# Kernel optimization log

Measured on AMD Instinct MI355X. Metric: run time of the kernel, lower is better.

The kernel has to match this reference:

```python
import jax, jax.numpy as jnp
import numpy as np

N_BLOCKS = 8
N_WIRES = 24
GAMMA, BETA, ALPHA = 0.1, 0.6, 0.15


def _apply_ry(state, w, theta):
    # RY(theta) = [[cos(t/2), -sin(t/2)], [sin(t/2), cos(t/2)]] on wire w.
    c = jnp.cos(theta * 0.5)
    s = jnp.sin(theta * 0.5)
    st = jnp.moveaxis(state, w, 0)  # (2, ...)
    new = jnp.stack([c * st[0] - s * st[1], s * st[0] + c * st[1]])
    return jnp.moveaxis(new, 0, w)


def _apply_cnot(state, ctrl, tgt):
    # Flip target bit where control bit == 1.
    st = jnp.moveaxis(state, (ctrl, tgt), (0, 1))  # (2, 2, ...)
    new = jnp.stack([st[0], st[1, ::-1]])
    return jnp.moveaxis(new, (0, 1), (ctrl, tgt))


def setup_inputs() -> dict:
    key = jax.random.key(0)
    angles = jax.random.normal(key, (N_BLOCKS, N_WIRES), dtype=jnp.float32)
    return {"angles": angles}


def reference(angles):
    n_blocks, n_wires = angles.shape  # static
    # Initial state |0...0>; RY and CNOT are real, so the state stays real.
    state = jnp.zeros((2,) * n_wires, dtype=angles.dtype).at[(0,) * n_wires].set(1.0)
    for k in range(n_blocks):
        for w in range(n_wires):
            state = _apply_ry(state, w, angles[k, w])
        for w in range(n_wires - 1):  # circular=False -> linear chain
            state = _apply_cnot(state, w, w + 1)
    probs = (state.reshape(-1) ** 2).reshape(2 ** n_wires, 1)  # |amp|^2
    easy_scale = 2.0 ** (n_wires - 1)
    x = (BETA * jnp.tanh(GAMMA * easy_scale * probs)) ** ALPHA
    return x - jnp.mean(x)
```

## Files before the change

kernel.cpp:

```cpp
#include <hip/hip_runtime.h>

#define NB 8
#define SSIZE (1u << 24)


__global__ void k_prep(const float* __restrict__ ang, float* __restrict__ ws) {
    int t = threadIdx.x;
    if (t == 0) ws[0] = 0.0f;
    if (t < NB * 24) {
        float a = 0.5f * ang[t];
        ws[64 + t]  = __builtin_cosf(a);
        ws[256 + t] = __builtin_sinf(a);
    }
}


__device__ __forceinline__ unsigned sw(unsigned f) {
    return f ^ (((f >> 3) ^ (f >> 5)) & 7u);
}

__device__ __forceinline__ void ry2(float& a0, float& a1, float c, float s, bool ctl) {
    float w0 = c * a0 - s * a1;
    float w1 = s * a0 + c * a1;
    a0 = ctl ? w1 : w0;
    a1 = ctl ? w0 : w1;
}

template<int TB, int MODE>
__device__ __forceinline__ void stage16(float4* x, float c, float s) {
#pragma unroll
    for (int j0 = 0; j0 < 16; ++j0) {
        if (j0 & (1 << TB)) continue;
        const int j1 = j0 | (1 << TB);
        const bool ctl = (MODE == 1) || (MODE == 0 && ((j0 >> (TB + 1)) & 1));
        ry2(x[j0].x, x[j1].x, c, s, ctl);
        ry2(x[j0].y, x[j1].y, c, s, ctl);
        ry2(x[j0].z, x[j1].z, c, s, ctl);
        ry2(x[j0].w, x[j1].w, c, s, ctl);
    }
}

__device__ __forceinline__ void dstages(float4* x, float c1, float s1,
                                        float c0, float s0) {
#pragma unroll
    for (int j = 0; j < 16; ++j) {
        bool ctl = j & 1;
        ry2(x[j].x, x[j].z, c1, s1, ctl);
        ry2(x[j].y, x[j].w, c1, s1, ctl);
        ry2(x[j].x, x[j].y, c0, s0, false);
        ry2(x[j].z, x[j].w, c0, s0, true);
    }
}

__device__ __forceinline__ float xform(float v) {
    float z = 838860.8f * v * v;
    float e2 = __builtin_amdgcn_exp2f(z * 2.8853900817779268f);
    float big = 1.0f - 2.0f * __builtin_amdgcn_rcpf(e2 + 1.0f);
    float z2 = z * z;
    float small_ = z * (1.0f - 0.33333333f * z2 * (1.0f - 0.4f * z2));
    float t = (z < 0.04f) ? small_ : big;
    return __builtin_amdgcn_exp2f(0.15f * __builtin_amdgcn_logf(0.6f * t));
}

__global__ __launch_bounds__(256, 2) void k_passA(float* __restrict__ st,
                                                  float* __restrict__ ws,
                                                  int k, int fuse) {
    __shared__ float4 T4[4096];
    const unsigned m = blockIdx.x;
    const unsigned tid = threadIdx.x;
    const float* C = ws + 64 + k * 24;
    const float* S = ws + 256 + k * 24;
    float ca[14], sa[14];
#pragma unroll
    for (int b = 0; b < 14; ++b) { ca[b] = C[23 - b]; sa[b] = S[23 - b]; }

    float4* G4 = reinterpret_cast<float4*>(st) + (m << 12);
    float4 x[16];

#pragma unroll
    for (int jj = 0; jj < 16; ++jj) x[jj] = G4[tid + (jj << 8)];
    if (m & 1u) stage16<3, 1>(x, ca[13], sa[13]);
    else        stage16<3,-1>(x, ca[13], sa[13]);
    stage16<2, 0>(x, ca[12], sa[12]);
    stage16<1, 0>(x, ca[11], sa[11]);
    stage16<0, 0>(x, ca[10], sa[10]);
#pragma unroll
    for (int jj = 0; jj < 16; ++jj) T4[sw(tid | (jj << 8))] = x[jj];
    __syncthreads();
    {
        const unsigned fb = (tid & 31) | ((tid >> 5) << 9);
#pragma unroll
        for (int jj = 0; jj < 16; ++jj) x[jj] = T4[sw(fb | (jj << 5))];
        stage16<2, 0>(x, ca[9], sa[9]);
        stage16<1, 0>(x, ca[8], sa[8]);
        stage16<0, 0>(x, ca[7], sa[7]);
#pragma unroll
        for (int jj = 0; jj < 16; ++jj) T4[sw(fb | (jj << 5))] = x[jj];
    }
    __syncthreads();
    {
        const unsigned fb = (tid & 3) | ((tid >> 2) << 6);
#pragma unroll
        for (int jj = 0; jj < 16; ++jj) x[jj] = T4[sw(fb | (jj << 2))];
        stage16<2, 0>(x, ca[6], sa[6]);
        stage16<1, 0>(x, ca[5], sa[5]);
        stage16<0, 0>(x, ca[4], sa[4]);
#pragma unroll
        for (int jj = 0; jj < 16; ++jj) T4[sw(fb | (jj << 2))] = x[jj];
    }
    __syncthreads();
    {
#pragma unroll
        for (int jj = 0; jj < 16; ++jj)
            x[jj] = T4[sw((jj & 7) | (tid << 3) | ((jj >> 3) << 11))];
        stage16<1, 0>(x, ca[3], sa[3]);
        stage16<0, 0>(x, ca[2], sa[2]);
        dstages(x, ca[1], sa[1], ca[0], sa[0]);
        if (fuse) {
            float lsum = 0.f;
#pragma unroll
            for (int jj = 0; jj < 16; ++jj) {
                float* v = &x[jj].x;
#pragma unroll
                for (int d = 0; d < 4; ++d) { v[d] = xform(v[d]); lsum += v[d]; }
            }
#pragma unroll
            for (int jj = 0; jj < 16; ++jj)
                G4[(jj & 7) | (tid << 3) | ((jj >> 3) << 11)] = x[jj];
#pragma unroll
            for (int o = 32; o > 0; o >>= 1) lsum += __shfl_down(lsum, o, 64);
            __syncthreads();
            float* wsum = reinterpret_cast<float*>(T4);
            if ((tid & 63u) == 0) wsum[tid >> 6] = lsum;
            __syncthreads();
            if (tid == 0)
                atomicAdd(ws, wsum[0] + wsum[1] + wsum[2] + wsum[3]);
        } else {
#pragma unroll
            for (int jj = 0; jj < 16; ++jj)
                G4[(jj & 7) | (tid << 3) | ((jj >> 3) << 11)] = x[jj];
        }
    }
}

__global__ __launch_bounds__(256, 2) void k_passB(float* __restrict__ st,
                                                  const float* __restrict__ ws,
                                                  int k, int init) {
    __shared__ float4 T4[4096];
    const unsigned m = blockIdx.x;
    const unsigned tid = threadIdx.x;
    const float* C = ws + 64 + k * 24;
    const float* S = ws + 256 + k * 24;
    float cg[10], sg[10];
#pragma unroll
    for (int t = 0; t < 10; ++t) { cg[t] = C[9 - t]; sg[t] = S[9 - t]; }

    float4* G4 = reinterpret_cast<float4*>(st);
    const unsigned mb = m << 2;
    float4 x[16];

    if (init) {
        const float* C0 = ws + 64;
        const float* S0 = ws + 256;
        unsigned t2 = tid & 3u;
        unsigned th = tid >> 2;
        float P = 1.f;
        { unsigned g = (t2 ^ (t2 >> 1)) & 1u;      P *= g ? S0[21] : C0[21]; }
        { unsigned g = ((t2 >> 1) ^ m) & 1u;       P *= g ? S0[20] : C0[20]; }
#pragma unroll
        for (int b = 4; b <= 12; ++b) {
            unsigned g = ((m >> (b - 4)) ^ (m >> (b - 3))) & 1u;
            P *= g ? S0[23 - b] : C0[23 - b];
        }
        { unsigned g = ((m >> 9) ^ th) & 1u;       P *= g ? S0[10] : C0[10]; }
#pragma unroll
        for (int b = 14; b <= 18; ++b) {
            unsigned g = ((th >> (b - 14)) ^ (th >> (b - 13))) & 1u;
            P *= g ? S0[23 - b] : C0[23 - b];
        }
        float D[4];
#pragma unroll
        for (int d = 0; d < 4; ++d) {
            unsigned g0 = (d ^ (d >> 1)) & 1u;
            unsigned g1 = ((d >> 1) ^ t2) & 1u;
            D[d] = (g0 ? S0[23] : C0[23]) * (g1 ? S0[22] : C0[22]);
        }
        unsigned th5 = (th >> 5) & 1u;
#pragma unroll
        for (int jj = 0; jj < 16; ++jj) {
            unsigned g19 = (th5 ^ (unsigned)jj) & 1u;
            unsigned g20 = ((unsigned)jj ^ ((unsigned)jj >> 1)) & 1u;
            unsigned g21 = (((unsigned)jj >> 1) ^ ((unsigned)jj >> 2)) & 1u;
            unsigned g22 = (((unsigned)jj >> 2) ^ ((unsigned)jj >> 3)) & 1u;
            unsigned g23 = ((unsigned)jj >> 3) & 1u;
            float J = (g19 ? S0[4] : C0[4]) * (g20 ? S0[3] : C0[3]) *
                      (g21 ? S0[2] : C0[2]) * (g22 ? S0[1] : C0[1]) *
                      (g23 ? S0[0] : C0[0]);
            float PJ = P * J;
            x[jj] = make_float4(PJ * D[0], PJ * D[1], PJ * D[2], PJ * D[3]);
        }
    } else {
#pragma unroll
        for (int jj = 0; jj < 16; ++jj) {
            unsigned lf = tid | (jj << 8);
            x[jj] = G4[((lf >> 2) << 12) | mb | (lf & 3u)];
        }
    }
    stage16<3,-1>(x, cg[9], sg[9]);
    stage16<2, 0>(x, cg[8], sg[8]);
    stage16<1, 0>(x, cg[7], sg[7]);
    stage16<0, 0>(x, cg[6], sg[6]);
#pragma unroll
    for (int jj = 0; jj < 16; ++jj) T4[sw(tid | (jj << 8))] = x[jj];
    __syncthreads();
    {
        const unsigned fb = (tid & 31) | ((tid >> 5) << 9);
#pragma unroll
        for (int jj = 0; jj < 16; ++jj) x[jj] = T4[sw(fb | (jj << 5))];
        stage16<2, 0>(x, cg[5], sg[5]);
        stage16<1, 0>(x, cg[4], sg[4]);
        stage16<0, 0>(x, cg[3], sg[3]);
#pragma unroll
        for (int jj = 0; jj < 16; ++jj) T4[sw(fb | (jj << 5))] = x[jj];
    }
    __syncthreads();
    {
        const unsigned fb = (tid & 3) | ((tid >> 2) << 6);
#pragma unroll
        for (int jj = 0; jj < 16; ++jj) x[jj] = T4[sw(fb | (jj << 2))];
        stage16<2, 0>(x, cg[2], sg[2]);
        stage16<1, 0>(x, cg[1], sg[1]);
        stage16<0, 0>(x, cg[0], sg[0]);
#pragma unroll
        for (int jj = 0; jj < 16; ++jj) {
            unsigned lf = fb | (jj << 2);
            G4[((lf >> 2) << 12) | mb | (lf & 3u)] = x[jj];
        }
    }
}

__global__ void k_final(float* __restrict__ st, const float* __restrict__ ws) {
    unsigned idx = blockIdx.x * blockDim.x + threadIdx.x;
    unsigned stride = gridDim.x * blockDim.x;
    float mean = ws[0] * (1.0f / 16777216.0f);
    float4* G4 = reinterpret_cast<float4*>(st);
    for (unsigned q = idx; q < (SSIZE / 4); q += stride) {
        float4 v = G4[q];
        v.x -= mean; v.y -= mean; v.z -= mean; v.w -= mean;
        G4[q] = v;
    }
}

extern "C" void kernel_launch(void* const* d_in, const int* in_sizes, int n_in,
                              void* d_out, int out_size, void* d_ws, size_t ws_size,
                              hipStream_t stream) {
    const float* ang = (const float*)d_in[0];
    float* st = (float*)d_out;
    float* ws = (float*)d_ws;

    k_prep<<<1, 256, 0, stream>>>(ang, ws);
    for (int k = 1; k < NB; ++k) {
        k_passB<<<1024, 256, 0, stream>>>(st, ws, k, (k == 1) ? 1 : 0);
        k_passA<<<1024, 256, 0, stream>>>(st, ws, k, (k == NB - 1) ? 1 : 0);
    }
    k_final<<<4096, 256, 0, stream>>>(st, ws);
}
```

Baseline: 613.1 us.

## Use 512-thread blocks with cross-lane shuffle stages instead of LDS transposes

Each pass now runs 512 threads per block, each holding 8 float4 instead of 16. Most of the former shared-memory transpose rounds are replaced by wave-level __shfl_xor butterfly stages, with per-lane coefficients encoding the RY and CNOT permutation. This cuts LDS traffic and __syncthreads barriers and lowers register pressure to raise occupancy. The cost is many more shuffle instructions and more complex index and coefficient bookkeeping.

```diff
diff --git a/kernel.cpp b/kernel.cpp
--- a/kernel.cpp
+++ b/kernel.cpp
@@ -27,9 +27,9 @@
 }
 
 template<int TB, int MODE>
-__device__ __forceinline__ void stage16(float4* x, float c, float s) {
-#pragma unroll
-    for (int j0 = 0; j0 < 16; ++j0) {
+__device__ __forceinline__ void stage8(float4* x, float c, float s) {
+#pragma unroll
+    for (int j0 = 0; j0 < 8; ++j0) {
         if (j0 & (1 << TB)) continue;
         const int j1 = j0 | (1 << TB);
         const bool ctl = (MODE == 1) || (MODE == 0 && ((j0 >> (TB + 1)) & 1));
@@ -40,13 +40,51 @@
     }
 }
 
-__device__ __forceinline__ void dstages(float4* x, float c1, float s1,
+__device__ __forceinline__ void coefs(unsigned lane, int lb, bool g,
+                                      float c, float s, float& cA, float& cP) {
+    bool b = (lane >> lb) & 1u;
+    cA = g ? (b ? -s : s) : c;
+    cP = g ? c : (b ? s : -s);
+}
+
+__device__ __forceinline__ void lane_stage(float4* x, int mask, float cA, float cP) {
+#pragma unroll
+    for (int j = 0; j < 8; ++j) {
+        float px = __shfl_xor(x[j].x, mask, 64);
+        float py = __shfl_xor(x[j].y, mask, 64);
+        float pz = __shfl_xor(x[j].z, mask, 64);
+        float pw = __shfl_xor(x[j].w, mask, 64);
+        x[j].x = cA * x[j].x + cP * px;
+        x[j].y = cA * x[j].y + cP * py;
+        x[j].z = cA * x[j].z + cP * pz;
+        x[j].w = cA * x[j].w + cP * pw;
+    }
+}
+
+__device__ __forceinline__ void lane_stage_jc(float4* x, int mask,
+                                              float cA0, float cP0,
+                                              float cA1, float cP1) {
+#pragma unroll
+    for (int j = 0; j < 8; ++j) {
+        float cA = (j & 1) ? cA1 : cA0;
+        float cP = (j & 1) ? cP1 : cP0;
+        float px = __shfl_xor(x[j].x, mask, 64);
+        float py = __shfl_xor(x[j].y, mask, 64);
+        float pz = __shfl_xor(x[j].z, mask, 64);
+        float pw = __shfl_xor(x[j].w, mask, 64);
+        x[j].x = cA * x[j].x + cP * px;
+        x[j].y = cA * x[j].y + cP * py;
+        x[j].z = cA * x[j].z + cP * pz;
+        x[j].w = cA * x[j].w + cP * pw;
+    }
+}
+
+__device__ __forceinline__ void dstages(float4* x, float c1, float s1, bool g1,
                                         float c0, float s0) {
 #pragma unroll
-    for (int j = 0; j < 16; ++j) {
-        bool ctl = j & 1;
-        ry2(x[j].x, x[j].z, c1, s1, ctl);
-        ry2(x[j].y, x[j].w, c1, s1, ctl);
+    for (int j = 0; j < 8; ++j) {
+        ry2(x[j].x, x[j].z, c1, s1, g1);
+        ry2(x[j].y, x[j].w, c1, s1, g1);
         ry2(x[j].x, x[j].y, c0, s0, false);
         ry2(x[j].z, x[j].w, c0, s0, true);
     }
@@ -62,12 +100,13 @@
     return __builtin_amdgcn_exp2f(0.15f * __builtin_amdgcn_logf(0.6f * t));
 }
 
-__global__ __launch_bounds__(256, 2) void k_passA(float* __restrict__ st,
+__global__ __launch_bounds__(512, 4) void k_passA(float* __restrict__ st,
                                                   float* __restrict__ ws,
                                                   int k, int fuse) {
     __shared__ float4 T4[4096];
     const unsigned m = blockIdx.x;
     const unsigned tid = threadIdx.x;
+    const unsigned lane = tid & 63u;
     const float* C = ws + 64 + k * 24;
     const float* S = ws + 256 + k * 24;
     float ca[14], sa[14];
@@ -75,80 +114,72 @@
     for (int b = 0; b < 14; ++b) { ca[b] = C[23 - b]; sa[b] = S[23 - b]; }
 
     float4* G4 = reinterpret_cast<float4*>(st) + (m << 12);
-    float4 x[16];
-
-#pragma unroll
-    for (int jj = 0; jj < 16; ++jj) x[jj] = G4[tid + (jj << 8)];
-    if (m & 1u) stage16<3, 1>(x, ca[13], sa[13]);
-    else        stage16<3,-1>(x, ca[13], sa[13]);
-    stage16<2, 0>(x, ca[12], sa[12]);
-    stage16<1, 0>(x, ca[11], sa[11]);
-    stage16<0, 0>(x, ca[10], sa[10]);
-#pragma unroll
-    for (int jj = 0; jj < 16; ++jj) T4[sw(tid | (jj << 8))] = x[jj];
+    float4 x[8];
+
+#pragma unroll
+    for (int jj = 0; jj < 8; ++jj) x[jj] = G4[tid + (jj << 9)];
+    if (m & 1u) stage8<2, 1>(x, ca[13], sa[13]);
+    else        stage8<2,-1>(x, ca[13], sa[13]);
+    stage8<1, 0>(x, ca[12], sa[12]);
+    stage8<0, 0>(x, ca[11], sa[11]);
+#pragma unroll
+    for (int jj = 0; jj < 8; ++jj) T4[sw(tid | (jj << 9))] = x[jj];
     __syncthreads();
+    const unsigned hi = (tid >> 6) << 9;
+#pragma unroll
+    for (int jj = 0; jj < 8; ++jj) x[jj] = T4[sw(lane | (jj << 6) | hi)];
+    if (tid & 64u) stage8<2, 1>(x, ca[10], sa[10]);
+    else           stage8<2,-1>(x, ca[10], sa[10]);
+    stage8<1, 0>(x, ca[9], sa[9]);
+    stage8<0, 0>(x, ca[8], sa[8]);
     {
-        const unsigned fb = (tid & 31) | ((tid >> 5) << 9);
-#pragma unroll
-        for (int jj = 0; jj < 16; ++jj) x[jj] = T4[sw(fb | (jj << 5))];
-        stage16<2, 0>(x, ca[9], sa[9]);
-        stage16<1, 0>(x, ca[8], sa[8]);
-        stage16<0, 0>(x, ca[7], sa[7]);
-#pragma unroll
-        for (int jj = 0; jj < 16; ++jj) T4[sw(fb | (jj << 5))] = x[jj];
-    }
-    __syncthreads();
-    {
-        const unsigned fb = (tid & 3) | ((tid >> 2) << 6);
-#pragma unroll
-        for (int jj = 0; jj < 16; ++jj) x[jj] = T4[sw(fb | (jj << 2))];
-        stage16<2, 0>(x, ca[6], sa[6]);
-        stage16<1, 0>(x, ca[5], sa[5]);
-        stage16<0, 0>(x, ca[4], sa[4]);
-#pragma unroll
-        for (int jj = 0; jj < 16; ++jj) T4[sw(fb | (jj << 2))] = x[jj];
-    }
-    __syncthreads();
-    {
-#pragma unroll
-        for (int jj = 0; jj < 16; ++jj)
-            x[jj] = T4[sw((jj & 7) | (tid << 3) | ((jj >> 3) << 11))];
-        stage16<1, 0>(x, ca[3], sa[3]);
-        stage16<0, 0>(x, ca[2], sa[2]);
-        dstages(x, ca[1], sa[1], ca[0], sa[0]);
-        if (fuse) {
-            float lsum = 0.f;
-#pragma unroll
-            for (int jj = 0; jj < 16; ++jj) {
-                float* v = &x[jj].x;
-#pragma unroll
-                for (int d = 0; d < 4; ++d) { v[d] = xform(v[d]); lsum += v[d]; }
-            }
-#pragma unroll
-            for (int jj = 0; jj < 16; ++jj)
-                G4[(jj & 7) | (tid << 3) | ((jj >> 3) << 11)] = x[jj];
-#pragma unroll
-            for (int o = 32; o > 0; o >>= 1) lsum += __shfl_down(lsum, o, 64);
-            __syncthreads();
-            float* wsum = reinterpret_cast<float*>(T4);
-            if ((tid & 63u) == 0) wsum[tid >> 6] = lsum;
-            __syncthreads();
-            if (tid == 0)
-                atomicAdd(ws, wsum[0] + wsum[1] + wsum[2] + wsum[3]);
-        } else {
-#pragma unroll
-            for (int jj = 0; jj < 16; ++jj)
-                G4[(jj & 7) | (tid << 3) | ((jj >> 3) << 11)] = x[jj];
-        }
-    }
-}
-
-__global__ __launch_bounds__(256, 2) void k_passB(float* __restrict__ st,
+        float cA0, cP0, cA1, cP1;
+        coefs(lane, 5, false, ca[7], sa[7], cA0, cP0);
+        coefs(lane, 5, true,  ca[7], sa[7], cA1, cP1);
+        lane_stage_jc(x, 32, cA0, cP0, cA1, cP1);
+    }
+    { float cA, cP; coefs(lane, 4, (lane >> 5) & 1, ca[6], sa[6], cA, cP); lane_stage(x, 16, cA, cP); }
+    { float cA, cP; coefs(lane, 3, (lane >> 4) & 1, ca[5], sa[5], cA, cP); lane_stage(x,  8, cA, cP); }
+    { float cA, cP; coefs(lane, 2, (lane >> 3) & 1, ca[4], sa[4], cA, cP); lane_stage(x,  4, cA, cP); }
+    { float cA, cP; coefs(lane, 1, (lane >> 2) & 1, ca[3], sa[3], cA, cP); lane_stage(x,  2, cA, cP); }
+    { float cA, cP; coefs(lane, 0, (lane >> 1) & 1, ca[2], sa[2], cA, cP); lane_stage(x,  1, cA, cP); }
+    dstages(x, ca[1], sa[1], lane & 1u, ca[0], sa[0]);
+
+    if (fuse) {
+        float lsum = 0.f;
+#pragma unroll
+        for (int jj = 0; jj < 8; ++jj) {
+            float* v = &x[jj].x;
+#pragma unroll
+            for (int d = 0; d < 4; ++d) { v[d] = xform(v[d]); lsum += v[d]; }
+        }
+#pragma unroll
+        for (int jj = 0; jj < 8; ++jj) G4[lane | (jj << 6) | hi] = x[jj];
+#pragma unroll
+        for (int o = 32; o > 0; o >>= 1) lsum += __shfl_down(lsum, o, 64);
+        __syncthreads();
+        float* wsum = reinterpret_cast<float*>(T4);
+        if ((tid & 63u) == 0) wsum[tid >> 6] = lsum;
+        __syncthreads();
+        if (tid == 0) {
+            float b = 0.f;
+#pragma unroll
+            for (int i = 0; i < 8; ++i) b += wsum[i];
+            atomicAdd(ws, b);
+        }
+    } else {
+#pragma unroll
+        for (int jj = 0; jj < 8; ++jj) G4[lane | (jj << 6) | hi] = x[jj];
+    }
+}
+
+__global__ __launch_bounds__(512, 4) void k_passB(float* __restrict__ st,
                                                   const float* __restrict__ ws,
                                                   int k, int init) {
     __shared__ float4 T4[4096];
     const unsigned m = blockIdx.x;
     const unsigned tid = threadIdx.x;
+    const unsigned lane = tid & 63u;
     const float* C = ws + 64 + k * 24;
     const float* S = ws + 256 + k * 24;
     float cg[10], sg[10];
@@ -157,85 +188,77 @@
 
     float4* G4 = reinterpret_cast<float4*>(st);
     const unsigned mb = m << 2;
-    float4 x[16];
+    float4 x[8];
 
     if (init) {
         const float* C0 = ws + 64;
         const float* S0 = ws + 256;
-        unsigned t2 = tid & 3u;
-        unsigned th = tid >> 2;
         float P = 1.f;
-        { unsigned g = (t2 ^ (t2 >> 1)) & 1u;      P *= g ? S0[21] : C0[21]; }
-        { unsigned g = ((t2 >> 1) ^ m) & 1u;       P *= g ? S0[20] : C0[20]; }
+        { unsigned g = (tid ^ (tid >> 1)) & 1u;        P *= g ? S0[21] : C0[21]; }
+        { unsigned g = ((tid >> 1) ^ m) & 1u;          P *= g ? S0[20] : C0[20]; }
 #pragma unroll
         for (int b = 4; b <= 12; ++b) {
             unsigned g = ((m >> (b - 4)) ^ (m >> (b - 3))) & 1u;
             P *= g ? S0[23 - b] : C0[23 - b];
         }
-        { unsigned g = ((m >> 9) ^ th) & 1u;       P *= g ? S0[10] : C0[10]; }
-#pragma unroll
-        for (int b = 14; b <= 18; ++b) {
-            unsigned g = ((th >> (b - 14)) ^ (th >> (b - 13))) & 1u;
+        { unsigned g = ((m >> 9) ^ (tid >> 2)) & 1u;   P *= g ? S0[10] : C0[10]; }
+#pragma unroll
+        for (int b = 14; b <= 19; ++b) {
+            unsigned g = ((tid >> (b - 12)) ^ (tid >> (b - 11))) & 1u;
             P *= g ? S0[23 - b] : C0[23 - b];
         }
         float D[4];
 #pragma unroll
         for (int d = 0; d < 4; ++d) {
             unsigned g0 = (d ^ (d >> 1)) & 1u;
-            unsigned g1 = ((d >> 1) ^ t2) & 1u;
+            unsigned g1 = ((d >> 1) ^ tid) & 1u;
             D[d] = (g0 ? S0[23] : C0[23]) * (g1 ? S0[22] : C0[22]);
         }
-        unsigned th5 = (th >> 5) & 1u;
-#pragma unroll
-        for (int jj = 0; jj < 16; ++jj) {
-            unsigned g19 = (th5 ^ (unsigned)jj) & 1u;
-            unsigned g20 = ((unsigned)jj ^ ((unsigned)jj >> 1)) & 1u;
-            unsigned g21 = (((unsigned)jj >> 1) ^ ((unsigned)jj >> 2)) & 1u;
-            unsigned g22 = (((unsigned)jj >> 2) ^ ((unsigned)jj >> 3)) & 1u;
-            unsigned g23 = ((unsigned)jj >> 3) & 1u;
-            float J = (g19 ? S0[4] : C0[4]) * (g20 ? S0[3] : C0[3]) *
-                      (g21 ? S0[2] : C0[2]) * (g22 ? S0[1] : C0[1]) *
-                      (g23 ? S0[0] : C0[0]);
+        unsigned t8 = (tid >> 8) & 1u;
+#pragma unroll
+        for (int jj = 0; jj < 8; ++jj) {
+            unsigned g20 = (t8 ^ (unsigned)jj) & 1u;
+            unsigned g21 = ((unsigned)jj ^ ((unsigned)jj >> 1)) & 1u;
+            unsigned g22 = (((unsigned)jj >> 1) ^ ((unsigned)jj >> 2)) & 1u;
+            unsigned g23 = (((unsigned)jj >> 2)) & 1u;
+            float J = (g20 ? S0[3] : C0[3]) * (g21 ? S0[2] : C0[2]) *
+                      (g22 ? S0[1] : C0[1]) * (g23 ? S0[0] : C0[0]);
             float PJ = P * J;
             x[jj] = make_float4(PJ * D[0], PJ * D[1], PJ * D[2], PJ * D[3]);
         }
     } else {
 #pragma unroll
-        for (int jj = 0; jj < 16; ++jj) {
-            unsigned lf = tid | (jj << 8);
-            x[jj] = G4[((lf >> 2) << 12) | mb | (lf & 3u)];
-        }
-    }
-    stage16<3,-1>(x, cg[9], sg[9]);
-    stage16<2, 0>(x, cg[8], sg[8]);
-    stage16<1, 0>(x, cg[7], sg[7]);
-    stage16<0, 0>(x, cg[6], sg[6]);
-#pragma unroll
-    for (int jj = 0; jj < 16; ++jj) T4[sw(tid | (jj << 8))] = x[jj];
+        for (int jj = 0; jj < 8; ++jj) {
+            unsigned lf = tid | (jj << 9);
+            x[jj] = G4[(lf & 3u) | mb | ((lf >> 2) << 12)];
+        }
+    }
+    stage8<2,-1>(x, cg[9], sg[9]);
+    stage8<1, 0>(x, cg[8], sg[8]);
+    stage8<0, 0>(x, cg[7], sg[7]);
+#pragma unroll
+    for (int jj = 0; jj < 8; ++jj) T4[sw(tid | (jj << 9))] = x[jj];
     __syncthreads();
+    const unsigned hi = (tid >> 6) << 9;
+#pragma unroll
+    for (int jj = 0; jj < 8; ++jj) x[jj] = T4[sw(lane | (jj << 6) | hi)];
+    if (tid & 64u) stage8<2, 1>(x, cg[6], sg[6]);
+    else           stage8<2,-1>(x, cg[6], sg[6]);
+    stage8<1, 0>(x, cg[5], sg[5]);
+    stage8<0, 0>(x, cg[4], sg[4]);
     {
-        const unsigned fb = (tid & 31) | ((tid >> 5) << 9);
-#pragma unroll
-        for (int jj = 0; jj < 16; ++jj) x[jj] = T4[sw(fb | (jj << 5))];
-        stage16<2, 0>(x, cg[5], sg[5]);
-        stage16<1, 0>(x, cg[4], sg[4]);
-        stage16<0, 0>(x, cg[3], sg[3]);
-#pragma unroll
-        for (int jj = 0; jj < 16; ++jj) T4[sw(fb | (jj << 5))] = x[jj];
-    }
-    __syncthreads();
-    {
-        const unsigned fb = (tid & 3) | ((tid >> 2) << 6);
-#pragma unroll
-        for (int jj = 0; jj < 16; ++jj) x[jj] = T4[sw(fb | (jj << 2))];
-        stage16<2, 0>(x, cg[2], sg[2]);
-        stage16<1, 0>(x, cg[1], sg[1]);
-        stage16<0, 0>(x, cg[0], sg[0]);
-#pragma unroll
-        for (int jj = 0; jj < 16; ++jj) {
-            unsigned lf = fb | (jj << 2);
-            G4[((lf >> 2) << 12) | mb | (lf & 3u)] = x[jj];
-        }
+        float cA0, cP0, cA1, cP1;
+        coefs(lane, 5, false, cg[3], sg[3], cA0, cP0);
+        coefs(lane, 5, true,  cg[3], sg[3], cA1, cP1);
+        lane_stage_jc(x, 32, cA0, cP0, cA1, cP1);
+    }
+    { float cA, cP; coefs(lane, 4, (lane >> 5) & 1, cg[2], sg[2], cA, cP); lane_stage(x, 16, cA, cP); }
+    { float cA, cP; coefs(lane, 3, (lane >> 4) & 1, cg[1], sg[1], cA, cP); lane_stage(x,  8, cA, cP); }
+    { float cA, cP; coefs(lane, 2, (lane >> 3) & 1, cg[0], sg[0], cA, cP); lane_stage(x,  4, cA, cP); }
+#pragma unroll
+    for (int jj = 0; jj < 8; ++jj) {
+        unsigned lf = lane | (jj << 6) | hi;
+        G4[(lf & 3u) | mb | ((lf >> 2) << 12)] = x[jj];
     }
 }
 
@@ -260,8 +283,8 @@
 
     k_prep<<<1, 256, 0, stream>>>(ang, ws);
     for (int k = 1; k < NB; ++k) {
-        k_passB<<<1024, 256, 0, stream>>>(st, ws, k, (k == 1) ? 1 : 0);
-        k_passA<<<1024, 256, 0, stream>>>(st, ws, k, (k == NB - 1) ? 1 : 0);
+        k_passB<<<1024, 512, 0, stream>>>(st, ws, k, (k == 1) ? 1 : 0);
+        k_passA<<<1024, 512, 0, stream>>>(st, ws, k, (k == NB - 1) ? 1 : 0);
     }
     k_final<<<4096, 256, 0, stream>>>(st, ws);
 }
```

Result: faster. 530.7 us (-13.4%).
